# Kernel tuning notes

Measured on AMD Instinct MI355X. Metric: run time of the kernel, lower is better.

The kernel has to match this reference:

```python
import jax, jax.numpy as jnp
import numpy as np

# dims: B frames, L residues, E embed, C comp_size, K kernel, NL layers, V vocab
B, L, E, C, K, NL, V = 64, 256, 128, 16, 5, 4, 21
STEP = 0.1


def setup_inputs() -> dict:
    key = jax.random.key(0)
    ks = jax.random.split(key, 9)
    aa_array = jax.random.randint(ks[0], (B, L), 0, V)
    bb_coords = jax.random.normal(ks[1], (B, L, 3), dtype=jnp.float32)
    emb = jax.random.normal(ks[2], (V, E), dtype=jnp.float32) * 0.05
    conv_w = jax.random.normal(ks[3], (NL, E, E, K), dtype=jnp.float32) * (1.0 / np.sqrt(E * K))
    conv_b = jax.random.normal(ks[4], (NL, E), dtype=jnp.float32) * 0.01
    t1_w = jax.random.normal(ks[5], (E * C, E), dtype=jnp.float32) * (1.0 / np.sqrt(E))
    t1_b = jax.random.normal(ks[6], (E * C,), dtype=jnp.float32) * 0.01
    t2_w = jax.random.normal(ks[7], (3 * C, 3), dtype=jnp.float32) * (1.0 / np.sqrt(3.0))
    t2_b = jax.random.normal(ks[8], (3 * C,), dtype=jnp.float32) * 0.01
    return {"aa_array": aa_array, "bb_coords": bb_coords, "emb": emb,
            "conv_w": conv_w, "conv_b": conv_b,
            "t1_w": t1_w, "t1_b": t1_b, "t2_w": t2_w, "t2_b": t2_b}


def _forward(aa_array, bb_coords, emb, conv_w, conv_b, t1_w, t1_b, t2_w, t2_b):
    # --- model.call: embed + residual conv stack with tanh ---
    h = emb[aa_array].transpose(0, 2, 1)  # (B, E, L)
    for i in range(NL):
        y = jax.lax.conv_general_dilated(
            h, conv_w[i], window_strides=(1,), padding='SAME',
            dimension_numbers=('NCH', 'OIH', 'NCH'))
        h = jnp.tanh(h + y + conv_b[i][None, :, None])
    x = h.transpose(0, 2, 1)  # (B, L, E)

    # --- pairwise coordinate message passing ---
    xx = bb_coords[:, :, None] - bb_coords[:, None, :]        # (B, L, L, 3)
    x2 = (x @ t1_w.T + t1_b).reshape(B, L, E, C)              # (B, L, E, C)
    # xc[b,c,i,j] = sum_e x[b,i,e] * x2[b,j,e,c]
    scores = jnp.einsum('bie,bjec->bcij', x, x2)              # (B, C, L, L)
    sm = jax.nn.softmax(scores, axis=1)                       # softmax over C

    # torch: pv = t2(xx).reshape(B,L,L,3,C); vd[b,a,k] = sum_{d,c} pv[b,a,d,k,c]*sm[b,c,d,a]
    # fused form (same math, avoids materializing pv of shape (B,L,L,3,C)):
    W2 = t2_w.reshape(3, C, 3)   # (k, c, m)
    b2 = t2_b.reshape(3, C)      # (k, c)
    s = jnp.einsum('badm,bcda->bcam', xx, sm)                 # (B, C, L, 3)
    vd = (jnp.einsum('kcm,bcam->bak', W2, s)
          + jnp.einsum('kc,bca->bak', b2, sm.sum(axis=2)))    # (B, L, 3)

    new_bb = bb_coords + STEP * vd
    mse = jnp.square(new_bb[1:] - bb_coords[:-1]).sum(-1).mean(1)  # (B-1,)
    return mse


def reference(aa_array, bb_coords, emb, conv_w, conv_b, t1_w, t1_b, t2_w, t2_b):
    return _forward(aa_array, bb_coords, emb, conv_w, conv_b, t1_w, t1_b, t2_w, t2_b)
```

## Files before the change

### kernel.cpp

```cpp
#include <hip/hip_runtime.h>

#define B_ 64
#define L_ 256
#define E_ 128
#define C_ 16
#define K_ 5
#define NL_ 4
#define STEP_ 0.1f
#define LOG2E_ 1.4426950408889634f

typedef __bf16 bfh;
typedef __attribute__((ext_vector_type(8))) __bf16 bf16x8;
typedef __attribute__((ext_vector_type(4))) float f32x4;
typedef __attribute__((ext_vector_type(16))) float f32x16;

#define SWZ(r) (((r) ^ ((r) >> 4)) & 15)

#if __has_builtin(__builtin_amdgcn_exp2f)
#define EXP2(x) __builtin_amdgcn_exp2f(x)
#else
static __device__ __forceinline__ float EXP2(float x) {
  float r;
  asm("v_exp_f32 %0, %1\n\ts_nop 0" : "=v"(r) : "v"(x));
  return r;
}
#endif

__global__ void k_prep_w(const float* __restrict__ w, bfh* __restrict__ wT) {
  int i = blockIdx.x * 256 + threadIdx.x;
  if (i >= NL_ * K_ * E_ * E_) return;
  int ii = i & 127;
  int rest = i >> 7;
  int o = rest & 127;
  int rest2 = rest >> 7;
  int k = rest2 % K_;
  int lay = rest2 / K_;
  wT[i] = (bfh)w[(((size_t)lay * E_ + o) * E_ + ii) * K_ + k];
}

__global__ void k_prep_t1(const float* __restrict__ t1w, bfh* __restrict__ t1wb) {
  int i = blockIdx.x * 256 + threadIdx.x;
  if (i < 2048 * 128) t1wb[i] = (bfh)(t1w[i] * LOG2E_);
}

__global__ __launch_bounds__(512, 4) void k_conv0(const int* __restrict__ aa,
                                                  const float* __restrict__ emb,
                                                  const bfh* __restrict__ wT,
                                                  const float* __restrict__ bias,
                                                  bfh* __restrict__ xout) {
  __shared__ __align__(16) char hs[36 * 256];
  const int b = blockIdx.y;
  const int lb = blockIdx.x * 32;
  const int t = threadIdx.x;

  for (int s = t; s < 36 * 16; s += 512) {
    int row = s >> 4, ch = s & 15;
    int lp = lb + row - 2;
    uint4 pk = {0, 0, 0, 0};
    if (lp >= 0 && lp < L_) {
      int idx = aa[b * L_ + lp];
      float4 f0 = *(const float4*)(emb + (size_t)idx * E_ + ch * 8);
      float4 f1 = *(const float4*)(emb + (size_t)idx * E_ + ch * 8 + 4);
      union { bfh h[8]; uint4 u; } cv;
      cv.h[0] = (bfh)f0.x; cv.h[1] = (bfh)f0.y; cv.h[2] = (bfh)f0.z; cv.h[3] = (bfh)f0.w;
      cv.h[4] = (bfh)f1.x; cv.h[5] = (bfh)f1.y; cv.h[6] = (bfh)f1.z; cv.h[7] = (bfh)f1.w;
      pk = cv.u;
    }
    *(uint4*)(hs + row * 256 + ((ch ^ (row & 7)) << 4)) = pk;
  }
  __syncthreads();

  const int wv = t >> 6, lane = t & 63;
  const int c16 = lane & 15, kg = lane >> 4;
  const int msub = wv & 1;
  const int nq = wv >> 1;

#pragma unroll
  for (int ntl = 0; ntl < 2; ++ntl) {
    const int n0 = nq * 32 + ntl * 16;
    f32x4 acc = {0.f, 0.f, 0.f, 0.f};
#pragma unroll
    for (int k = 0; k < K_; ++k) {
      const bfh* bp = wT + ((size_t)(k * E_ + n0 + c16)) * E_ + kg * 8;
      bf16x8 b0 = *(const bf16x8*)(bp);
      bf16x8 b1 = *(const bf16x8*)(bp + 32);
      bf16x8 b2 = *(const bf16x8*)(bp + 64);
      bf16x8 b3 = *(const bf16x8*)(bp + 96);
      const int row = msub * 16 + c16 + k;
      bf16x8 a0 = *(const bf16x8*)(hs + row * 256 + (((0 * 4 + kg) ^ (row & 7)) << 4));
      bf16x8 a1 = *(const bf16x8*)(hs + row * 256 + (((1 * 4 + kg) ^ (row & 7)) << 4));
      bf16x8 a2 = *(const bf16x8*)(hs + row * 256 + (((2 * 4 + kg) ^ (row & 7)) << 4));
      bf16x8 a3 = *(const bf16x8*)(hs + row * 256 + (((3 * 4 + kg) ^ (row & 7)) << 4));
      acc = __builtin_amdgcn_mfma_f32_16x16x32_bf16(a0, b0, acc, 0, 0, 0);
      acc = __builtin_amdgcn_mfma_f32_16x16x32_bf16(a1, b1, acc, 0, 0, 0);
      acc = __builtin_amdgcn_mfma_f32_16x16x32_bf16(a2, b2, acc, 0, 0, 0);
      acc = __builtin_amdgcn_mfma_f32_16x16x32_bf16(a3, b3, acc, 0, 0, 0);
    }
    const int o = n0 + c16;
    const float bo = bias[o];
#pragma unroll
    for (int r = 0; r < 4; ++r) {
      int lrow = msub * 16 + kg * 4 + r;
      int srow = lrow + 2;
      float res = (float)*(const bfh*)(hs + srow * 256 +
                                       (((o >> 3) ^ (srow & 7)) << 4) + (o & 7) * 2);
      float v = acc[r] + res + bo;
      float ex = EXP2(2.f * LOG2E_ * v);
      float th = 1.f - 2.f / (ex + 1.f);
      xout[((size_t)b * L_ + lb + lrow) * E_ + o] = (bfh)th;
    }
  }
}

__global__ __launch_bounds__(512, 4) void k_conv(const bfh* __restrict__ xin,
                                                 const bfh* __restrict__ wT,
                                                 const float* __restrict__ bias,
                                                 bfh* __restrict__ xout) {
  __shared__ __align__(16) char hs[36 * 256];
  const int b = blockIdx.y;
  const int lb = blockIdx.x * 32;
  const int t = threadIdx.x;

  for (int s = t; s < 36 * 16; s += 512) {
    int row = s >> 4, ch = s & 15;
    int lp = lb + row - 2;
    uint4 z = {0, 0, 0, 0};
    uint4 v = (lp >= 0 && lp < L_)
                  ? *(const uint4*)(xin + ((size_t)b * L_ + lp) * E_ + ch * 8)
                  : z;
    *(uint4*)(hs + row * 256 + ((ch ^ (row & 7)) << 4)) = v;
  }
  __syncthreads();

  const int wv = t >> 6, lane = t & 63;
  const int c16 = lane & 15, kg = lane >> 4;
  const int msub = wv & 1;
  const int nq = wv >> 1;

#pragma unroll
  for (int ntl = 0; ntl < 2; ++ntl) {
    const int n0 = nq * 32 + ntl * 16;
    f32x4 acc = {0.f, 0.f, 0.f, 0.f};
#pragma unroll
    for (int k = 0; k < K_; ++k) {
      const bfh* bp = wT + ((size_t)(k * E_ + n0 + c16)) * E_ + kg * 8;
      bf16x8 b0 = *(const bf16x8*)(bp);
      bf16x8 b1 = *(const bf16x8*)(bp + 32);
      bf16x8 b2 = *(const bf16x8*)(bp + 64);
      bf16x8 b3 = *(const bf16x8*)(bp + 96);
      const int row = msub * 16 + c16 + k;
      bf16x8 a0 = *(const bf16x8*)(hs + row * 256 + (((0 * 4 + kg) ^ (row & 7)) << 4));
      bf16x8 a1 = *(const bf16x8*)(hs + row * 256 + (((1 * 4 + kg) ^ (row & 7)) << 4));
      bf16x8 a2 = *(const bf16x8*)(hs + row * 256 + (((2 * 4 + kg) ^ (row & 7)) << 4));
      bf16x8 a3 = *(const bf16x8*)(hs + row * 256 + (((3 * 4 + kg) ^ (row & 7)) << 4));
      acc = __builtin_amdgcn_mfma_f32_16x16x32_bf16(a0, b0, acc, 0, 0, 0);
      acc = __builtin_amdgcn_mfma_f32_16x16x32_bf16(a1, b1, acc, 0, 0, 0);
      acc = __builtin_amdgcn_mfma_f32_16x16x32_bf16(a2, b2, acc, 0, 0, 0);
      acc = __builtin_amdgcn_mfma_f32_16x16x32_bf16(a3, b3, acc, 0, 0, 0);
    }
    const int o = n0 + c16;
    const float bo = bias[o];
#pragma unroll
    for (int r = 0; r < 4; ++r) {
      int lrow = msub * 16 + kg * 4 + r;
      int srow = lrow + 2;
      float res = (float)*(const bfh*)(hs + srow * 256 +
                                       (((o >> 3) ^ (srow & 7)) << 4) + (o & 7) * 2);
      float v = acc[r] + res + bo;
      float ex = EXP2(2.f * LOG2E_ * v);
      float th = 1.f - 2.f / (ex + 1.f);
      xout[((size_t)b * L_ + lb + lrow) * E_ + o] = (bfh)th;
    }
  }
}

__global__ __launch_bounds__(512, 4) void k_conv_last(const bfh* __restrict__ xin,
                                                      const bfh* __restrict__ wT,
                                                      const float* __restrict__ bias,
                                                      bfh* __restrict__ xTg) {
  __shared__ __align__(16) char hs[36 * 256];
  const int b = blockIdx.y;
  const int lb = blockIdx.x * 32;
  const int dt = blockIdx.x;
  const int t = threadIdx.x;

  for (int s = t; s < 36 * 16; s += 512) {
    int row = s >> 4, ch = s & 15;
    int lp = lb + row - 2;
    uint4 z = {0, 0, 0, 0};
    uint4 v = (lp >= 0 && lp < L_)
                  ? *(const uint4*)(xin + ((size_t)b * L_ + lp) * E_ + ch * 8)
                  : z;
    *(uint4*)(hs + row * 256 + ((ch ^ (row & 7)) << 4)) = v;
  }
  __syncthreads();

  const int wv = t >> 6, lane = t & 63;
  const int c16 = lane & 15, kg = lane >> 4;
  const int msub = wv & 1;
  const int nq = wv >> 1;

#pragma unroll
  for (int ntl = 0; ntl < 2; ++ntl) {
    const int n0 = nq * 32 + ntl * 16;
    f32x4 acc = {0.f, 0.f, 0.f, 0.f};
#pragma unroll
    for (int k = 0; k < K_; ++k) {
      const bfh* bp = wT + ((size_t)(k * E_ + n0 + c16)) * E_ + kg * 8;
      bf16x8 b0 = *(const bf16x8*)(bp);
      bf16x8 b1 = *(const bf16x8*)(bp + 32);
      bf16x8 b2 = *(const bf16x8*)(bp + 64);
      bf16x8 b3 = *(const bf16x8*)(bp + 96);
      const int row = msub * 16 + c16 + k;
      bf16x8 a0 = *(const bf16x8*)(hs + row * 256 + (((0 * 4 + kg) ^ (row & 7)) << 4));
      bf16x8 a1 = *(const bf16x8*)(hs + row * 256 + (((1 * 4 + kg) ^ (row & 7)) << 4));
      bf16x8 a2 = *(const bf16x8*)(hs + row * 256 + (((2 * 4 + kg) ^ (row & 7)) << 4));
      bf16x8 a3 = *(const bf16x8*)(hs + row * 256 + (((3 * 4 + kg) ^ (row & 7)) << 4));
      acc = __builtin_amdgcn_mfma_f32_16x16x32_bf16(a0, b0, acc, 0, 0, 0);
      acc = __builtin_amdgcn_mfma_f32_16x16x32_bf16(a1, b1, acc, 0, 0, 0);
      acc = __builtin_amdgcn_mfma_f32_16x16x32_bf16(a2, b2, acc, 0, 0, 0);
      acc = __builtin_amdgcn_mfma_f32_16x16x32_bf16(a3, b3, acc, 0, 0, 0);
    }
    const int o = n0 + c16;
    const int kkp = nq * 2 + ntl;
    const int hic = c16 >> 3;
    const int e7 = c16 & 7;
    const float bo = bias[o];
#pragma unroll
    for (int r = 0; r < 4; ++r) {
      int lrow = msub * 16 + kg * 4 + r;
      int srow = lrow + 2;
      float res = (float)*(const bfh*)(hs + srow * 256 +
                                       (((o >> 3) ^ (srow & 7)) << 4) + (o & 7) * 2);
      float v = acc[r] + res + bo;
      float ex = EXP2(2.f * LOG2E_ * v);
      float th = 1.f - 2.f / (ex + 1.f);
      size_t el = ((((size_t)b * 8 + dt) * 8 + kkp) * 2 + hic) * 256 + lrow * 8 + e7;
      xTg[el] = (bfh)th;
    }
  }
}

__global__ __launch_bounds__(512, 2) void k_x2(const bfh* __restrict__ xTg,
                                               const bfh* __restrict__ t1wb,
                                               const float* __restrict__ t1b,
                                               bfh* __restrict__ x2g,
                                               int bBase) {
  __shared__ __align__(16) char smem[65536 + 2 * 8192];
  char* XF = smem;
  const unsigned u = blockIdx.x;
  const int xcd = u & 7;
  const int g = u >> 3;
  const int b_loc = xcd + 8 * (g >> 3);
  const int ne = g & 7;
  const int b = bBase + b_loc;
  const int t = threadIdx.x;
  const int wv = t >> 6, lane = t & 63;
  const int c16 = lane & 15, kg = lane >> 4;

#pragma unroll
  for (int i = 0; i < 8; ++i) {
    int c = t + i * 512;
    int l31 = c & 31, hi5 = (c >> 5) & 1, kk = (c >> 6) & 7, dt = c >> 9;
    int row = dt * 32 + l31;
    int ch = (kk * 2 + hi5) ^ SWZ(row);
    *(uint4*)(XF + row * 256 + (ch << 4)) =
        *(const uint4*)(xTg + (size_t)b * 32768 + (size_t)c * 8);
  }
  __syncthreads();

  bf16x8 bf[2][4];
  float bias[2];
#pragma unroll
  for (int j = 0; j < 2; ++j) {
    const int e = ne * 16 + wv * 2 + j;
    const int n = e * 16 + c16;
#pragma unroll
    for (int kk = 0; kk < 4; ++kk)
      bf[j][kk] = *(const bf16x8*)(t1wb + (size_t)n * 128 + kk * 32 + kg * 8);
    bias[j] = t1b[n] * LOG2E_;
  }

#pragma unroll 1
  for (int st = 0; st < 16; ++st) {
    char* sc = smem + 65536 + (st & 1) * 8192;
    bf16x8 a1[4];
    const int rowa = st * 16 + c16;
#pragma unroll
    for (int kk = 0; kk < 4; ++kk)
      a1[kk] = *(const bf16x8*)(XF + rowa * 256 + (((kk * 4 + kg) ^ SWZ(rowa)) << 4));
    f32x4 acc0 = {0.f, 0.f, 0.f, 0.f};
    f32x4 acc1 = {0.f, 0.f, 0.f, 0.f};
#pragma unroll
    for (int kk = 0; kk < 4; ++kk) {
      acc0 = __builtin_amdgcn_mfma_f32_16x16x32_bf16(a1[kk], bf[0][kk], acc0, 0, 0, 0);
      acc1 = __builtin_amdgcn_mfma_f32_16x16x32_bf16(a1[kk], bf[1][kk], acc1, 0, 0, 0);
    }
#pragma unroll
    for (int r = 0; r < 4; ++r) {
      int a = kg * 4 + r;
      int m5 = (c16 & 3) | ((a & 1) << 2) | ((c16 >> 2) << 3);
      int row = (a >> 1) * 32 + m5;
      union { bfh h; ushort s; } lo, hi2;
      lo.h = (bfh)(acc0[r] + bias[0]);
      hi2.h = (bfh)(acc1[r] + bias[1]);
      unsigned pk = (unsigned)lo.s | ((unsigned)hi2.s << 16);
      *(unsigned*)(sc + row * 32 + (((wv) ^ ((row >> 2) & 7)) << 2)) = pk;
    }
    __syncthreads();
    {
      const int m32 = t & 31;
      const int eo = (t >> 5) & 1;
      const int mb = t >> 6;
      const int row = mb * 32 + m32;
      uint4 v;
      unsigned* vp = (unsigned*)&v;
#pragma unroll
      for (int jj = 0; jj < 4; ++jj) {
        int j2 = eo * 4 + jj;
        vp[jj] = *(const unsigned*)(sc + row * 32 + ((j2 ^ ((row >> 2) & 7)) << 2));
      }
      size_t el = (((size_t)(b_loc * 128 + st * 8 + mb)) * 16 + ne * 2 + eo) * 256 + m32 * 8;
      *(uint4*)(x2g + el) = v;
    }
  }
}

__global__ __launch_bounds__(512, 2) void k_pair(
    const bfh* __restrict__ xTg,
    const float* __restrict__ bb,
    const bfh* __restrict__ x2g,
    const float* __restrict__ t2w,
    const float* __restrict__ t2b,
    float* __restrict__ vkp,
    int bBase) {
  __shared__ __align__(16) float bbs[L_ * 3];
  const int t = threadIdx.x;
  const unsigned u = blockIdx.x;
  const int b_loc = (u & 7) | ((u >> 8) << 3);
  const int inner = (u >> 3) & 31;
  const int atile = inner >> 1;
  const int dh = inner & 1;
  const int b = bBase + b_loc;
  const int lane = t & 63;
  const int wv = t >> 6;
  const int l31 = lane & 31;
  const int hi = lane >> 5;

  if (t < 192) ((float4*)bbs)[t] = ((const float4*)(bb + b * (L_ * 3)))[t];
  __syncthreads();

  bf16x8 afr[8];
  const bfh* abase = x2g + ((size_t)(b_loc * 128 + atile * 8 + wv)) * 4096 + l31 * 8;
#pragma unroll
  for (int kk = 0; kk < 8; ++kk)
    afr[kk] = *(const bf16x8*)(abase + (kk * 2 + hi) * 256);

  const int aglob = atile * 16 + 2 * wv + hi;
  const float bax0 = bbs[aglob * 3 + 0];
  const float bax1 = bbs[aglob * 3 + 1];
  const float bax2 = bbs[aglob * 3 + 2];

  float accX[16], accY[16], accZ[16], accS[16];
#pragma unroll
  for (int q = 0; q < 16; ++q) { accX[q] = 0.f; accY[q] = 0.f; accZ[q] = 0.f; accS[q] = 0.f; }

  const bfh* xb = xTg + (size_t)b * 32768 + hi * 256 + l31 * 8;
  bf16x8 bcur[8], bnxt[8];
#pragma unroll
  for (int kk = 0; kk < 8; ++kk)
    bcur[kk] = *(const bf16x8*)(xb + (size_t)(dh * 4) * 4096 + kk * 512);

#pragma unroll
  for (int dt = 0; dt < 4; ++dt) {
    const int dtg = dh * 4 + dt;
    if (dt < 3) {
#pragma unroll
      for (int kk = 0; kk < 8; ++kk)
        bnxt[kk] = *(const bf16x8*)(xb + (size_t)(dtg + 1) * 4096 + kk * 512);
    }
    f32x16 acc;
#pragma unroll
    for (int q = 0; q < 16; ++q) acc[q] = 0.f;
#pragma unroll
    for (int kk = 0; kk < 8; ++kk)
      acc = __builtin_amdgcn_mfma_f32_32x32x16_bf16(afr[kk], bcur[kk], acc, 0, 0, 0);
    const int d = dtg * 32 + l31;
    const float dx = bax0 - bbs[d * 3 + 0];
    const float dy = bax1 - bbs[d * 3 + 1];
    const float dz = bax2 - bbs[d * 3 + 2];
    float p[16];
#pragma unroll
    for (int q = 0; q < 16; ++q) p[q] = EXP2(acc[q]);
    const float s0 = (p[0] + p[1]) + (p[2] + p[3]);
    const float s1 = (p[4] + p[5]) + (p[6] + p[7]);
    const float s2 = (p[8] + p[9]) + (p[10] + p[11]);
    const float s3 = (p[12] + p[13]) + (p[14] + p[15]);
    const float S = (s0 + s1) + (s2 + s3);
    const float inv = __builtin_amdgcn_rcpf(S);
    const float dxn = dx * inv, dyn = dy * inv, dzn = dz * inv;
#pragma unroll
    for (int q = 0; q < 16; ++q) {
      accS[q] = fmaf(p[q], inv, accS[q]);
      accX[q] = fmaf(p[q], dxn, accX[q]);
      accY[q] = fmaf(p[q], dyn, accY[q]);
      accZ[q] = fmaf(p[q], dzn, accZ[q]);
    }
#pragma unroll
    for (int kk = 0; kk < 8; ++kk) bcur[kk] = bnxt[kk];
  }

  float vk[3] = {0.f, 0.f, 0.f};
#pragma unroll
  for (int c = 0; c < 16; ++c) {
#pragma unroll
    for (int k = 0; k < 3; ++k) {
      const float* w2 = t2w + (k * C_ + c) * 3;
      vk[k] += w2[0] * accX[c] + w2[1] * accY[c] + w2[2] * accZ[c] +
               t2b[k * C_ + c] * accS[c];
    }
  }
#pragma unroll
  for (int m = 1; m <= 16; m <<= 1) {
    vk[0] += __shfl_xor(vk[0], m);
    vk[1] += __shfl_xor(vk[1], m);
    vk[2] += __shfl_xor(vk[2], m);
  }
  if (l31 == 0) {
#pragma unroll
    for (int k = 0; k < 3; ++k)
      vkp[(((size_t)b * 2 + dh) * L_ + aglob) * 3 + k] = vk[k];
  }
}

__global__ void k_mse(const float* __restrict__ vkp, const float* __restrict__ bb,
                      float* __restrict__ out) {
  const int b = blockIdx.x;
  const int t = threadIdx.x;
  const int bp1 = b + 1;
  float v = 0.f;
#pragma unroll
  for (int k = 0; k < 3; ++k) {
    float vd = vkp[(((size_t)bp1 * 2 + 0) * L_ + t) * 3 + k] +
               vkp[(((size_t)bp1 * 2 + 1) * L_ + t) * 3 + k];
    float nb = bb[((size_t)bp1 * L_ + t) * 3 + k] + STEP_ * vd;
    float d = nb - bb[((size_t)b * L_ + t) * 3 + k];
    v += d * d;
  }
  for (int o = 32; o > 0; o >>= 1) v += __shfl_down(v, o);
  __shared__ float wsum[4];
  if ((t & 63) == 0) wsum[t >> 6] = v;
  __syncthreads();
  if (t == 0) out[b] = (wsum[0] + wsum[1] + wsum[2] + wsum[3]) * (1.0f / L_);
}

extern "C" void kernel_launch(void* const* d_in, const int* in_sizes, int n_in,
                              void* d_out, int out_size, void* d_ws, size_t ws_size,
                              hipStream_t stream) {
  const int* aa = (const int*)d_in[0];
  const float* bb = (const float*)d_in[1];
  const float* emb = (const float*)d_in[2];
  const float* conv_w = (const float*)d_in[3];
  const float* conv_b = (const float*)d_in[4];
  const float* t1w = (const float*)d_in[5];
  const float* t1b = (const float*)d_in[6];
  const float* t2w = (const float*)d_in[7];
  const float* t2b = (const float*)d_in[8];
  float* out = (float*)d_out;

  char* ws = (char*)d_ws;
  bfh* xA = (bfh*)ws;
  bfh* xTg = (bfh*)(ws + 4194304);
  bfh* t1wb = (bfh*)(ws + 8388608);
  bfh* wT = (bfh*)(ws + 8912896);
  float* vkp = (float*)(ws + 9568256);
  bfh* x2g = (bfh*)(ws + 10485760);
  bfh* xB = (bfh*)(ws + 10485760);

  k_prep_t1<<<1024, 256, 0, stream>>>(t1w, t1wb);
  k_prep_w<<<(NL_ * K_ * E_ * E_ + 255) / 256, 256, 0, stream>>>(conv_w, wT);

  k_conv0<<<dim3(L_ / 32, B_), 512, 0, stream>>>(aa, emb, wT + (size_t)0 * K_ * E_ * E_,
                                                 conv_b + 0 * E_, xB);
  k_conv<<<dim3(L_ / 32, B_), 512, 0, stream>>>(xB, wT + (size_t)1 * K_ * E_ * E_,
                                                conv_b + 1 * E_, xA);
  k_conv<<<dim3(L_ / 32, B_), 512, 0, stream>>>(xA, wT + (size_t)2 * K_ * E_ * E_,
                                                conv_b + 2 * E_, xB);
  k_conv_last<<<dim3(L_ / 32, B_), 512, 0, stream>>>(xB, wT + (size_t)3 * K_ * E_ * E_,
                                                     conv_b + 3 * E_, xTg);

  const size_t need1 = 10485760ull + 67108864ull;
  if (ws_size >= need1) {
    k_x2<<<B_ * 8, 512, 0, stream>>>(xTg, t1wb, t1b, x2g, 0);
    k_pair<<<B_ * 32, 512, 0, stream>>>(xTg, bb, x2g, t2w, t2b, vkp, 0);
  } else {
    for (int pass = 0; pass < 2; ++pass) {
      const int bBase = pass * 32;
      k_x2<<<32 * 8, 512, 0, stream>>>(xTg, t1wb, t1b, x2g, bBase);
      k_pair<<<32 * 32, 512, 0, stream>>>(xTg, bb, x2g, t2w, t2b, vkp, bBase);
    }
  }

  k_mse<<<B_ - 1, 256, 0, stream>>>(vkp, bb, out);
}
```

Baseline: 155.7 us.

## Fuse four conv layers into one kernel with halo recompute in LDS

Replaces the four per-layer conv kernels with a single kernel that loads a 48-row tile (8-row halo each side) and runs layers 0-2 entirely in shared memory, recomputing the halo rows. Only the final layer writes to global memory, in the transposed layout. This removes three global round-trips of activations and three kernel launches. The two weight-prep kernels are also merged into one launch. The cost is redundant halo computation (48 rows computed per 32 output rows), more LDS per block, and lower occupancy (launch bounds 2 instead of 4).

```diff
diff --git a/kernel.cpp b/kernel.cpp
--- a/kernel.cpp
+++ b/kernel.cpp
@@ -26,36 +26,42 @@
 }
 #endif
 
-__global__ void k_prep_w(const float* __restrict__ w, bfh* __restrict__ wT) {
+__global__ void k_prep(const float* __restrict__ w, const float* __restrict__ t1w,
+                       bfh* __restrict__ wT, bfh* __restrict__ t1wb) {
   int i = blockIdx.x * 256 + threadIdx.x;
-  if (i >= NL_ * K_ * E_ * E_) return;
-  int ii = i & 127;
-  int rest = i >> 7;
-  int o = rest & 127;
-  int rest2 = rest >> 7;
-  int k = rest2 % K_;
-  int lay = rest2 / K_;
-  wT[i] = (bfh)w[(((size_t)lay * E_ + o) * E_ + ii) * K_ + k];
-}
-
-__global__ void k_prep_t1(const float* __restrict__ t1w, bfh* __restrict__ t1wb) {
-  int i = blockIdx.x * 256 + threadIdx.x;
-  if (i < 2048 * 128) t1wb[i] = (bfh)(t1w[i] * LOG2E_);
-}
-
-__global__ __launch_bounds__(512, 4) void k_conv0(const int* __restrict__ aa,
+  const int NW = NL_ * K_ * E_ * E_;
+  if (i < NW) {
+    int ii = i & 127;
+    int rest = i >> 7;
+    int o = rest & 127;
+    int rest2 = rest >> 7;
+    int k = rest2 % K_;
+    int lay = rest2 / K_;
+    wT[i] = (bfh)w[(((size_t)lay * E_ + o) * E_ + ii) * K_ + k];
+    return;
+  }
+  int j = i - NW;
+  if (j < 2048 * 128) t1wb[j] = (bfh)(t1w[j] * LOG2E_);
+}
+
+__global__ __launch_bounds__(512, 2) void k_conv4(const int* __restrict__ aa,
                                                   const float* __restrict__ emb,
                                                   const bfh* __restrict__ wT,
-                                                  const float* __restrict__ bias,
-                                                  bfh* __restrict__ xout) {
-  __shared__ __align__(16) char hs[36 * 256];
+                                                  const float* __restrict__ conv_b,
+                                                  bfh* __restrict__ xTg) {
+  __shared__ __align__(16) char smem[3 * 12288];
+  char* bufIn = smem;
+  char* bufA = smem + 12288;
+  char* bufB = smem + 24576;
   const int b = blockIdx.y;
   const int lb = blockIdx.x * 32;
   const int t = threadIdx.x;
-
-  for (int s = t; s < 36 * 16; s += 512) {
+  const int wv = t >> 6, lane = t & 63;
+  const int c16 = lane & 15, kg = lane >> 4;
+
+  for (int s = t; s < 48 * 16; s += 512) {
     int row = s >> 4, ch = s & 15;
-    int lp = lb + row - 2;
+    int lp = lb + row - 8;
     uint4 pk = {0, 0, 0, 0};
     if (lp >= 0 && lp < L_) {
       int idx = aa[b * L_ + lp];
@@ -66,177 +72,102 @@
       cv.h[4] = (bfh)f1.x; cv.h[5] = (bfh)f1.y; cv.h[6] = (bfh)f1.z; cv.h[7] = (bfh)f1.w;
       pk = cv.u;
     }
-    *(uint4*)(hs + row * 256 + ((ch ^ (row & 7)) << 4)) = pk;
+    *(uint4*)(bufIn + row * 256 + ((ch ^ (row & 7)) << 4)) = pk;
   }
   __syncthreads();
 
-  const int wv = t >> 6, lane = t & 63;
-  const int c16 = lane & 15, kg = lane >> 4;
-  const int msub = wv & 1;
-  const int nq = wv >> 1;
-
-#pragma unroll
-  for (int ntl = 0; ntl < 2; ++ntl) {
-    const int n0 = nq * 32 + ntl * 16;
-    f32x4 acc = {0.f, 0.f, 0.f, 0.f};
-#pragma unroll
-    for (int k = 0; k < K_; ++k) {
-      const bfh* bp = wT + ((size_t)(k * E_ + n0 + c16)) * E_ + kg * 8;
-      bf16x8 b0 = *(const bf16x8*)(bp);
-      bf16x8 b1 = *(const bf16x8*)(bp + 32);
-      bf16x8 b2 = *(const bf16x8*)(bp + 64);
-      bf16x8 b3 = *(const bf16x8*)(bp + 96);
-      const int row = msub * 16 + c16 + k;
-      bf16x8 a0 = *(const bf16x8*)(hs + row * 256 + (((0 * 4 + kg) ^ (row & 7)) << 4));
-      bf16x8 a1 = *(const bf16x8*)(hs + row * 256 + (((1 * 4 + kg) ^ (row & 7)) << 4));
-      bf16x8 a2 = *(const bf16x8*)(hs + row * 256 + (((2 * 4 + kg) ^ (row & 7)) << 4));
-      bf16x8 a3 = *(const bf16x8*)(hs + row * 256 + (((3 * 4 + kg) ^ (row & 7)) << 4));
-      acc = __builtin_amdgcn_mfma_f32_16x16x32_bf16(a0, b0, acc, 0, 0, 0);
-      acc = __builtin_amdgcn_mfma_f32_16x16x32_bf16(a1, b1, acc, 0, 0, 0);
-      acc = __builtin_amdgcn_mfma_f32_16x16x32_bf16(a2, b2, acc, 0, 0, 0);
-      acc = __builtin_amdgcn_mfma_f32_16x16x32_bf16(a3, b3, acc, 0, 0, 0);
-    }
-    const int o = n0 + c16;
-    const float bo = bias[o];
-#pragma unroll
-    for (int r = 0; r < 4; ++r) {
-      int lrow = msub * 16 + kg * 4 + r;
-      int srow = lrow + 2;
-      float res = (float)*(const bfh*)(hs + srow * 256 +
-                                       (((o >> 3) ^ (srow & 7)) << 4) + (o & 7) * 2);
-      float v = acc[r] + res + bo;
-      float ex = EXP2(2.f * LOG2E_ * v);
-      float th = 1.f - 2.f / (ex + 1.f);
-      xout[((size_t)b * L_ + lb + lrow) * E_ + o] = (bfh)th;
-    }
-  }
-}
-
-__global__ __launch_bounds__(512, 4) void k_conv(const bfh* __restrict__ xin,
-                                                 const bfh* __restrict__ wT,
-                                                 const float* __restrict__ bias,
-                                                 bfh* __restrict__ xout) {
-  __shared__ __align__(16) char hs[36 * 256];
-  const int b = blockIdx.y;
-  const int lb = blockIdx.x * 32;
-  const int t = threadIdx.x;
-
-  for (int s = t; s < 36 * 16; s += 512) {
-    int row = s >> 4, ch = s & 15;
-    int lp = lb + row - 2;
-    uint4 z = {0, 0, 0, 0};
-    uint4 v = (lp >= 0 && lp < L_)
-                  ? *(const uint4*)(xin + ((size_t)b * L_ + lp) * E_ + ch * 8)
-                  : z;
-    *(uint4*)(hs + row * 256 + ((ch ^ (row & 7)) << 4)) = v;
-  }
-  __syncthreads();
-
-  const int wv = t >> 6, lane = t & 63;
-  const int c16 = lane & 15, kg = lane >> 4;
-  const int msub = wv & 1;
-  const int nq = wv >> 1;
-
-#pragma unroll
-  for (int ntl = 0; ntl < 2; ++ntl) {
-    const int n0 = nq * 32 + ntl * 16;
-    f32x4 acc = {0.f, 0.f, 0.f, 0.f};
-#pragma unroll
-    for (int k = 0; k < K_; ++k) {
-      const bfh* bp = wT + ((size_t)(k * E_ + n0 + c16)) * E_ + kg * 8;
-      bf16x8 b0 = *(const bf16x8*)(bp);
-      bf16x8 b1 = *(const bf16x8*)(bp + 32);
-      bf16x8 b2 = *(const bf16x8*)(bp + 64);
-      bf16x8 b3 = *(const bf16x8*)(bp + 96);
-      const int row = msub * 16 + c16 + k;
-      bf16x8 a0 = *(const bf16x8*)(hs + row * 256 + (((0 * 4 + kg) ^ (row & 7)) << 4));
-      bf16x8 a1 = *(const bf16x8*)(hs + row * 256 + (((1 * 4 + kg) ^ (row & 7)) << 4));
-      bf16x8 a2 = *(const bf16x8*)(hs + row * 256 + (((2 * 4 + kg) ^ (row & 7)) << 4));
-      bf16x8 a3 = *(const bf16x8*)(hs + row * 256 + (((3 * 4 + kg) ^ (row & 7)) << 4));
-      acc = __builtin_amdgcn_mfma_f32_16x16x32_bf16(a0, b0, acc, 0, 0, 0);
-      acc = __builtin_amdgcn_mfma_f32_16x16x32_bf16(a1, b1, acc, 0, 0, 0);
-      acc = __builtin_amdgcn_mfma_f32_16x16x32_bf16(a2, b2, acc, 0, 0, 0);
-      acc = __builtin_amdgcn_mfma_f32_16x16x32_bf16(a3, b3, acc, 0, 0, 0);
-    }
-    const int o = n0 + c16;
-    const float bo = bias[o];
-#pragma unroll
-    for (int r = 0; r < 4; ++r) {
-      int lrow = msub * 16 + kg * 4 + r;
-      int srow = lrow + 2;
-      float res = (float)*(const bfh*)(hs + srow * 256 +
-                                       (((o >> 3) ^ (srow & 7)) << 4) + (o & 7) * 2);
-      float v = acc[r] + res + bo;
-      float ex = EXP2(2.f * LOG2E_ * v);
-      float th = 1.f - 2.f / (ex + 1.f);
-      xout[((size_t)b * L_ + lb + lrow) * E_ + o] = (bfh)th;
-    }
-  }
-}
-
-__global__ __launch_bounds__(512, 4) void k_conv_last(const bfh* __restrict__ xin,
-                                                      const bfh* __restrict__ wT,
-                                                      const float* __restrict__ bias,
-                                                      bfh* __restrict__ xTg) {
-  __shared__ __align__(16) char hs[36 * 256];
-  const int b = blockIdx.y;
-  const int lb = blockIdx.x * 32;
-  const int dt = blockIdx.x;
-  const int t = threadIdx.x;
-
-  for (int s = t; s < 36 * 16; s += 512) {
-    int row = s >> 4, ch = s & 15;
-    int lp = lb + row - 2;
-    uint4 z = {0, 0, 0, 0};
-    uint4 v = (lp >= 0 && lp < L_)
-                  ? *(const uint4*)(xin + ((size_t)b * L_ + lp) * E_ + ch * 8)
-                  : z;
-    *(uint4*)(hs + row * 256 + ((ch ^ (row & 7)) << 4)) = v;
-  }
-  __syncthreads();
-
-  const int wv = t >> 6, lane = t & 63;
-  const int c16 = lane & 15, kg = lane >> 4;
-  const int msub = wv & 1;
-  const int nq = wv >> 1;
-
-#pragma unroll
-  for (int ntl = 0; ntl < 2; ++ntl) {
-    const int n0 = nq * 32 + ntl * 16;
-    f32x4 acc = {0.f, 0.f, 0.f, 0.f};
-#pragma unroll
-    for (int k = 0; k < K_; ++k) {
-      const bfh* bp = wT + ((size_t)(k * E_ + n0 + c16)) * E_ + kg * 8;
-      bf16x8 b0 = *(const bf16x8*)(bp);
-      bf16x8 b1 = *(const bf16x8*)(bp + 32);
-      bf16x8 b2 = *(const bf16x8*)(bp + 64);
-      bf16x8 b3 = *(const bf16x8*)(bp + 96);
-      const int row = msub * 16 + c16 + k;
-      bf16x8 a0 = *(const bf16x8*)(hs + row * 256 + (((0 * 4 + kg) ^ (row & 7)) << 4));
-      bf16x8 a1 = *(const bf16x8*)(hs + row * 256 + (((1 * 4 + kg) ^ (row & 7)) << 4));
-      bf16x8 a2 = *(const bf16x8*)(hs + row * 256 + (((2 * 4 + kg) ^ (row & 7)) << 4));
-      bf16x8 a3 = *(const bf16x8*)(hs + row * 256 + (((3 * 4 + kg) ^ (row & 7)) << 4));
-      acc = __builtin_amdgcn_mfma_f32_16x16x32_bf16(a0, b0, acc, 0, 0, 0);
-      acc = __builtin_amdgcn_mfma_f32_16x16x32_bf16(a1, b1, acc, 0, 0, 0);
-      acc = __builtin_amdgcn_mfma_f32_16x16x32_bf16(a2, b2, acc, 0, 0, 0);
-      acc = __builtin_amdgcn_mfma_f32_16x16x32_bf16(a3, b3, acc, 0, 0, 0);
-    }
-    const int o = n0 + c16;
-    const int kkp = nq * 2 + ntl;
-    const int hic = c16 >> 3;
-    const int e7 = c16 & 7;
-    const float bo = bias[o];
-#pragma unroll
-    for (int r = 0; r < 4; ++r) {
-      int lrow = msub * 16 + kg * 4 + r;
-      int srow = lrow + 2;
-      float res = (float)*(const bfh*)(hs + srow * 256 +
-                                       (((o >> 3) ^ (srow & 7)) << 4) + (o & 7) * 2);
-      float v = acc[r] + res + bo;
-      float ex = EXP2(2.f * LOG2E_ * v);
-      float th = 1.f - 2.f / (ex + 1.f);
-      size_t el = ((((size_t)b * 8 + dt) * 8 + kkp) * 2 + hic) * 256 + lrow * 8 + e7;
-      xTg[el] = (bfh)th;
+  const char* src = bufIn;
+  char* dst = bufA;
+#pragma unroll 1
+  for (int lay = 0; lay < 3; ++lay) {
+    const bfh* wL = wT + (size_t)lay * K_ * E_ * E_;
+    const float* bL = conv_b + lay * E_;
+#pragma unroll
+    for (int j = 0; j < 3; ++j) {
+      const int pi = wv * 3 + j;
+      const int ot = pi & 7, mt = pi >> 3;
+      const int o = ot * 16 + c16;
+      f32x4 acc = {0.f, 0.f, 0.f, 0.f};
+#pragma unroll
+      for (int k = 0; k < K_; ++k) {
+        const bfh* bp = wL + ((size_t)(k * E_ + o)) * E_ + kg * 8;
+        bf16x8 b0 = *(const bf16x8*)(bp);
+        bf16x8 b1 = *(const bf16x8*)(bp + 32);
+        bf16x8 b2 = *(const bf16x8*)(bp + 64);
+        bf16x8 b3 = *(const bf16x8*)(bp + 96);
+        int rt = mt * 16 + c16 + k - 2;
+        rt = rt < 0 ? 0 : (rt > 47 ? 47 : rt);
+        bf16x8 a0 = *(const bf16x8*)(src + rt * 256 + (((0 * 4 + kg) ^ (rt & 7)) << 4));
+        bf16x8 a1 = *(const bf16x8*)(src + rt * 256 + (((1 * 4 + kg) ^ (rt & 7)) << 4));
+        bf16x8 a2 = *(const bf16x8*)(src + rt * 256 + (((2 * 4 + kg) ^ (rt & 7)) << 4));
+        bf16x8 a3 = *(const bf16x8*)(src + rt * 256 + (((3 * 4 + kg) ^ (rt & 7)) << 4));
+        acc = __builtin_amdgcn_mfma_f32_16x16x32_bf16(a0, b0, acc, 0, 0, 0);
+        acc = __builtin_amdgcn_mfma_f32_16x16x32_bf16(a1, b1, acc, 0, 0, 0);
+        acc = __builtin_amdgcn_mfma_f32_16x16x32_bf16(a2, b2, acc, 0, 0, 0);
+        acc = __builtin_amdgcn_mfma_f32_16x16x32_bf16(a3, b3, acc, 0, 0, 0);
+      }
+      const float bo = bL[o];
+#pragma unroll
+      for (int r = 0; r < 4; ++r) {
+        int ro = mt * 16 + kg * 4 + r;
+        int gl = lb - 8 + ro;
+        float res = (float)*(const bfh*)(src + ro * 256 +
+                                         (((o >> 3) ^ (ro & 7)) << 4) + (o & 7) * 2);
+        float v = acc[r] + res + bo;
+        float ex = EXP2(2.f * LOG2E_ * v);
+        float th = 1.f - 2.f / (ex + 1.f);
+        if (gl < 0 || gl >= L_) th = 0.f;
+        *(bfh*)(dst + ro * 256 + (((o >> 3) ^ (ro & 7)) << 4) + (o & 7) * 2) = (bfh)th;
+      }
+    }
+    __syncthreads();
+    src = dst;
+    dst = (lay == 0) ? bufB : bufA;
+  }
+
+  {
+    const bfh* wL = wT + (size_t)3 * K_ * E_ * E_;
+    const float* bL = conv_b + 3 * E_;
+    const int msub = wv & 1;
+    const int nq = wv >> 1;
+#pragma unroll
+    for (int ntl = 0; ntl < 2; ++ntl) {
+      const int n0 = nq * 32 + ntl * 16;
+      const int o = n0 + c16;
+      f32x4 acc = {0.f, 0.f, 0.f, 0.f};
+#pragma unroll
+      for (int k = 0; k < K_; ++k) {
+        const bfh* bp = wL + ((size_t)(k * E_ + o)) * E_ + kg * 8;
+        bf16x8 b0 = *(const bf16x8*)(bp);
+        bf16x8 b1 = *(const bf16x8*)(bp + 32);
+        bf16x8 b2 = *(const bf16x8*)(bp + 64);
+        bf16x8 b3 = *(const bf16x8*)(bp + 96);
+        const int rt = msub * 16 + c16 + k + 6;
+        bf16x8 a0 = *(const bf16x8*)(src + rt * 256 + (((0 * 4 + kg) ^ (rt & 7)) << 4));
+        bf16x8 a1 = *(const bf16x8*)(src + rt * 256 + (((1 * 4 + kg) ^ (rt & 7)) << 4));
+        bf16x8 a2 = *(const bf16x8*)(src + rt * 256 + (((2 * 4 + kg) ^ (rt & 7)) << 4));
+        bf16x8 a3 = *(const bf16x8*)(src + rt * 256 + (((3 * 4 + kg) ^ (rt & 7)) << 4));
+        acc = __builtin_amdgcn_mfma_f32_16x16x32_bf16(a0, b0, acc, 0, 0, 0);
+        acc = __builtin_amdgcn_mfma_f32_16x16x32_bf16(a1, b1, acc, 0, 0, 0);
+        acc = __builtin_amdgcn_mfma_f32_16x16x32_bf16(a2, b2, acc, 0, 0, 0);
+        acc = __builtin_amdgcn_mfma_f32_16x16x32_bf16(a3, b3, acc, 0, 0, 0);
+      }
+      const float bo = bL[o];
+      const int kkp = nq * 2 + ntl;
+      const int hic = c16 >> 3;
+      const int e7 = c16 & 7;
+#pragma unroll
+      for (int r = 0; r < 4; ++r) {
+        int lrow = msub * 16 + kg * 4 + r;
+        int ro = lrow + 8;
+        float res = (float)*(const bfh*)(src + ro * 256 +
+                                         (((o >> 3) ^ (ro & 7)) << 4) + (o & 7) * 2);
+        float v = acc[r] + res + bo;
+        float ex = EXP2(2.f * LOG2E_ * v);
+        float th = 1.f - 2.f / (ex + 1.f);
+        size_t el = ((((size_t)b * 8 + blockIdx.x) * 8 + kkp) * 2 + hic) * 256 + lrow * 8 + e7;
+        xTg[el] = (bfh)th;
+      }
     }
   }
 }
@@ -469,25 +400,16 @@
   float* out = (float*)d_out;
 
   char* ws = (char*)d_ws;
-  bfh* xA = (bfh*)ws;
   bfh* xTg = (bfh*)(ws + 4194304);
   bfh* t1wb = (bfh*)(ws + 8388608);
   bfh* wT = (bfh*)(ws + 8912896);
   float* vkp = (float*)(ws + 9568256);
   bfh* x2g = (bfh*)(ws + 10485760);
-  bfh* xB = (bfh*)(ws + 10485760);
-
-  k_prep_t1<<<1024, 256, 0, stream>>>(t1w, t1wb);
-  k_prep_w<<<(NL_ * K_ * E_ * E_ + 255) / 256, 256, 0, stream>>>(conv_w, wT);
-
-  k_conv0<<<dim3(L_ / 32, B_), 512, 0, stream>>>(aa, emb, wT + (size_t)0 * K_ * E_ * E_,
-                                                 conv_b + 0 * E_, xB);
-  k_conv<<<dim3(L_ / 32, B_), 512, 0, stream>>>(xB, wT + (size_t)1 * K_ * E_ * E_,
-                                                conv_b + 1 * E_, xA);
-  k_conv<<<dim3(L_ / 32, B_), 512, 0, stream>>>(xA, wT + (size_t)2 * K_ * E_ * E_,
-                                                conv_b + 2 * E_, xB);
-  k_conv_last<<<dim3(L_ / 32, B_), 512, 0, stream>>>(xB, wT + (size_t)3 * K_ * E_ * E_,
-                                                     conv_b + 3 * E_, xTg);
+
+  const int NPREP = NL_ * K_ * E_ * E_ + 2048 * 128;
+  k_prep<<<(NPREP + 255) / 256, 256, 0, stream>>>(conv_w, t1w, wT, t1wb);
+
+  k_conv4<<<dim3(L_ / 32, B_), 512, 0, stream>>>(aa, emb, wT, conv_b, xTg);
 
   const size_t need1 = 10485760ull + 67108864ull;
   if (ws_size >= need1) {
```

Result: slower. 178.5 us (+14.7%).

## Halve conv row tiles, split accumulators, and merge weight prep kernels

Applied to the files above, without the earlier changes.

The conv kernels now cover 16 sequence rows per block instead of 32, which doubles the grid to 1024 blocks. Each wave owns one 16-channel output tile and alternates two independent MFMA accumulators, shortening the dependent MFMA chain. The two weight-prep kernels are merged into one launch. The trade-off is that each weight fragment is now reused over fewer rows, so weight traffic through L2 roughly doubles, and halo rows are reloaded more often.

```diff
diff --git a/kernel.cpp b/kernel.cpp
--- a/kernel.cpp
+++ b/kernel.cpp
@@ -26,35 +26,37 @@
 }
 #endif
 
-__global__ void k_prep_w(const float* __restrict__ w, bfh* __restrict__ wT) {
+__global__ void k_prep(const float* __restrict__ w, const float* __restrict__ t1w,
+                       bfh* __restrict__ wT, bfh* __restrict__ t1wb) {
   int i = blockIdx.x * 256 + threadIdx.x;
-  if (i >= NL_ * K_ * E_ * E_) return;
-  int ii = i & 127;
-  int rest = i >> 7;
-  int o = rest & 127;
-  int rest2 = rest >> 7;
-  int k = rest2 % K_;
-  int lay = rest2 / K_;
-  wT[i] = (bfh)w[(((size_t)lay * E_ + o) * E_ + ii) * K_ + k];
-}
-
-__global__ void k_prep_t1(const float* __restrict__ t1w, bfh* __restrict__ t1wb) {
-  int i = blockIdx.x * 256 + threadIdx.x;
-  if (i < 2048 * 128) t1wb[i] = (bfh)(t1w[i] * LOG2E_);
-}
+  const int NW = NL_ * K_ * E_ * E_;
+  if (i < NW) {
+    int ii = i & 127;
+    int rest = i >> 7;
+    int o = rest & 127;
+    int rest2 = rest >> 7;
+    int k = rest2 % K_;
+    int lay = rest2 / K_;
+    wT[i] = (bfh)w[(((size_t)lay * E_ + o) * E_ + ii) * K_ + k];
+    return;
+  }
+  int j = i - NW;
+  if (j < 2048 * 128) t1wb[j] = (bfh)(t1w[j] * LOG2E_);
+}
+
 
 __global__ __launch_bounds__(512, 4) void k_conv0(const int* __restrict__ aa,
                                                   const float* __restrict__ emb,
                                                   const bfh* __restrict__ wT,
                                                   const float* __restrict__ bias,
                                                   bfh* __restrict__ xout) {
-  __shared__ __align__(16) char hs[36 * 256];
+  __shared__ __align__(16) char hs[20 * 256];
   const int b = blockIdx.y;
-  const int lb = blockIdx.x * 32;
-  const int t = threadIdx.x;
-
-  for (int s = t; s < 36 * 16; s += 512) {
-    int row = s >> 4, ch = s & 15;
+  const int lb = blockIdx.x * 16;
+  const int t = threadIdx.x;
+
+  if (t < 20 * 16) {
+    int row = t >> 4, ch = t & 15;
     int lp = lb + row - 2;
     uint4 pk = {0, 0, 0, 0};
     if (lp >= 0 && lp < L_) {
@@ -72,43 +74,38 @@
 
   const int wv = t >> 6, lane = t & 63;
   const int c16 = lane & 15, kg = lane >> 4;
-  const int msub = wv & 1;
-  const int nq = wv >> 1;
-
-#pragma unroll
-  for (int ntl = 0; ntl < 2; ++ntl) {
-    const int n0 = nq * 32 + ntl * 16;
-    f32x4 acc = {0.f, 0.f, 0.f, 0.f};
-#pragma unroll
-    for (int k = 0; k < K_; ++k) {
-      const bfh* bp = wT + ((size_t)(k * E_ + n0 + c16)) * E_ + kg * 8;
-      bf16x8 b0 = *(const bf16x8*)(bp);
-      bf16x8 b1 = *(const bf16x8*)(bp + 32);
-      bf16x8 b2 = *(const bf16x8*)(bp + 64);
-      bf16x8 b3 = *(const bf16x8*)(bp + 96);
-      const int row = msub * 16 + c16 + k;
-      bf16x8 a0 = *(const bf16x8*)(hs + row * 256 + (((0 * 4 + kg) ^ (row & 7)) << 4));
-      bf16x8 a1 = *(const bf16x8*)(hs + row * 256 + (((1 * 4 + kg) ^ (row & 7)) << 4));
-      bf16x8 a2 = *(const bf16x8*)(hs + row * 256 + (((2 * 4 + kg) ^ (row & 7)) << 4));
-      bf16x8 a3 = *(const bf16x8*)(hs + row * 256 + (((3 * 4 + kg) ^ (row & 7)) << 4));
-      acc = __builtin_amdgcn_mfma_f32_16x16x32_bf16(a0, b0, acc, 0, 0, 0);
-      acc = __builtin_amdgcn_mfma_f32_16x16x32_bf16(a1, b1, acc, 0, 0, 0);
-      acc = __builtin_amdgcn_mfma_f32_16x16x32_bf16(a2, b2, acc, 0, 0, 0);
-      acc = __builtin_amdgcn_mfma_f32_16x16x32_bf16(a3, b3, acc, 0, 0, 0);
-    }
-    const int o = n0 + c16;
-    const float bo = bias[o];
-#pragma unroll
-    for (int r = 0; r < 4; ++r) {
-      int lrow = msub * 16 + kg * 4 + r;
-      int srow = lrow + 2;
-      float res = (float)*(const bfh*)(hs + srow * 256 +
-                                       (((o >> 3) ^ (srow & 7)) << 4) + (o & 7) * 2);
-      float v = acc[r] + res + bo;
-      float ex = EXP2(2.f * LOG2E_ * v);
-      float th = 1.f - 2.f / (ex + 1.f);
-      xout[((size_t)b * L_ + lb + lrow) * E_ + o] = (bfh)th;
-    }
+  const int o = wv * 16 + c16;
+
+  f32x4 acc0 = {0.f, 0.f, 0.f, 0.f};
+  f32x4 acc1 = {0.f, 0.f, 0.f, 0.f};
+#pragma unroll
+  for (int k = 0; k < K_; ++k) {
+    const bfh* bp = wT + ((size_t)(k * E_ + o)) * E_ + kg * 8;
+    bf16x8 b0 = *(const bf16x8*)(bp);
+    bf16x8 b1 = *(const bf16x8*)(bp + 32);
+    bf16x8 b2 = *(const bf16x8*)(bp + 64);
+    bf16x8 b3 = *(const bf16x8*)(bp + 96);
+    const int row = c16 + k;
+    bf16x8 a0 = *(const bf16x8*)(hs + row * 256 + (((0 * 4 + kg) ^ (row & 7)) << 4));
+    bf16x8 a1 = *(const bf16x8*)(hs + row * 256 + (((1 * 4 + kg) ^ (row & 7)) << 4));
+    bf16x8 a2 = *(const bf16x8*)(hs + row * 256 + (((2 * 4 + kg) ^ (row & 7)) << 4));
+    bf16x8 a3 = *(const bf16x8*)(hs + row * 256 + (((3 * 4 + kg) ^ (row & 7)) << 4));
+    acc0 = __builtin_amdgcn_mfma_f32_16x16x32_bf16(a0, b0, acc0, 0, 0, 0);
+    acc1 = __builtin_amdgcn_mfma_f32_16x16x32_bf16(a1, b1, acc1, 0, 0, 0);
+    acc0 = __builtin_amdgcn_mfma_f32_16x16x32_bf16(a2, b2, acc0, 0, 0, 0);
+    acc1 = __builtin_amdgcn_mfma_f32_16x16x32_bf16(a3, b3, acc1, 0, 0, 0);
+  }
+  const float bo = bias[o];
+#pragma unroll
+  for (int r = 0; r < 4; ++r) {
+    int lrow = kg * 4 + r;
+    int srow = lrow + 2;
+    float res = (float)*(const bfh*)(hs + srow * 256 +
+                                     (((o >> 3) ^ (srow & 7)) << 4) + (o & 7) * 2);
+    float v = acc0[r] + acc1[r] + res + bo;
+    float ex = EXP2(2.f * LOG2E_ * v);
+    float th = 1.f - 2.f / (ex + 1.f);
+    xout[((size_t)b * L_ + lb + lrow) * E_ + o] = (bfh)th;
   }
 }
 
@@ -116,13 +113,13 @@
                                                  const bfh* __restrict__ wT,
                                                  const float* __restrict__ bias,
                                                  bfh* __restrict__ xout) {
-  __shared__ __align__(16) char hs[36 * 256];
+  __shared__ __align__(16) char hs[20 * 256];
   const int b = blockIdx.y;
-  const int lb = blockIdx.x * 32;
-  const int t = threadIdx.x;
-
-  for (int s = t; s < 36 * 16; s += 512) {
-    int row = s >> 4, ch = s & 15;
+  const int lb = blockIdx.x * 16;
+  const int t = threadIdx.x;
+
+  if (t < 20 * 16) {
+    int row = t >> 4, ch = t & 15;
     int lp = lb + row - 2;
     uint4 z = {0, 0, 0, 0};
     uint4 v = (lp >= 0 && lp < L_)
@@ -134,43 +131,38 @@
 
   const int wv = t >> 6, lane = t & 63;
   const int c16 = lane & 15, kg = lane >> 4;
-  const int msub = wv & 1;
-  const int nq = wv >> 1;
-
-#pragma unroll
-  for (int ntl = 0; ntl < 2; ++ntl) {
-    const int n0 = nq * 32 + ntl * 16;
-    f32x4 acc = {0.f, 0.f, 0.f, 0.f};
-#pragma unroll
-    for (int k = 0; k < K_; ++k) {
-      const bfh* bp = wT + ((size_t)(k * E_ + n0 + c16)) * E_ + kg * 8;
-      bf16x8 b0 = *(const bf16x8*)(bp);
-      bf16x8 b1 = *(const bf16x8*)(bp + 32);
-      bf16x8 b2 = *(const bf16x8*)(bp + 64);
-      bf16x8 b3 = *(const bf16x8*)(bp + 96);
-      const int row = msub * 16 + c16 + k;
-      bf16x8 a0 = *(const bf16x8*)(hs + row * 256 + (((0 * 4 + kg) ^ (row & 7)) << 4));
-      bf16x8 a1 = *(const bf16x8*)(hs + row * 256 + (((1 * 4 + kg) ^ (row & 7)) << 4));
-      bf16x8 a2 = *(const bf16x8*)(hs + row * 256 + (((2 * 4 + kg) ^ (row & 7)) << 4));
-      bf16x8 a3 = *(const bf16x8*)(hs + row * 256 + (((3 * 4 + kg) ^ (row & 7)) << 4));
-      acc = __builtin_amdgcn_mfma_f32_16x16x32_bf16(a0, b0, acc, 0, 0, 0);
-      acc = __builtin_amdgcn_mfma_f32_16x16x32_bf16(a1, b1, acc, 0, 0, 0);
-      acc = __builtin_amdgcn_mfma_f32_16x16x32_bf16(a2, b2, acc, 0, 0, 0);
-      acc = __builtin_amdgcn_mfma_f32_16x16x32_bf16(a3, b3, acc, 0, 0, 0);
-    }
-    const int o = n0 + c16;
-    const float bo = bias[o];
-#pragma unroll
-    for (int r = 0; r < 4; ++r) {
-      int lrow = msub * 16 + kg * 4 + r;
-      int srow = lrow + 2;
-      float res = (float)*(const bfh*)(hs + srow * 256 +
-                                       (((o >> 3) ^ (srow & 7)) << 4) + (o & 7) * 2);
-      float v = acc[r] + res + bo;
-      float ex = EXP2(2.f * LOG2E_ * v);
-      float th = 1.f - 2.f / (ex + 1.f);
-      xout[((size_t)b * L_ + lb + lrow) * E_ + o] = (bfh)th;
-    }
+  const int o = wv * 16 + c16;
+
+  f32x4 acc0 = {0.f, 0.f, 0.f, 0.f};
+  f32x4 acc1 = {0.f, 0.f, 0.f, 0.f};
+#pragma unroll
+  for (int k = 0; k < K_; ++k) {
+    const bfh* bp = wT + ((size_t)(k * E_ + o)) * E_ + kg * 8;
+    bf16x8 b0 = *(const bf16x8*)(bp);
+    bf16x8 b1 = *(const bf16x8*)(bp + 32);
+    bf16x8 b2 = *(const bf16x8*)(bp + 64);
+    bf16x8 b3 = *(const bf16x8*)(bp + 96);
+    const int row = c16 + k;
+    bf16x8 a0 = *(const bf16x8*)(hs + row * 256 + (((0 * 4 + kg) ^ (row & 7)) << 4));
+    bf16x8 a1 = *(const bf16x8*)(hs + row * 256 + (((1 * 4 + kg) ^ (row & 7)) << 4));
+    bf16x8 a2 = *(const bf16x8*)(hs + row * 256 + (((2 * 4 + kg) ^ (row & 7)) << 4));
+    bf16x8 a3 = *(const bf16x8*)(hs + row * 256 + (((3 * 4 + kg) ^ (row & 7)) << 4));
+    acc0 = __builtin_amdgcn_mfma_f32_16x16x32_bf16(a0, b0, acc0, 0, 0, 0);
+    acc1 = __builtin_amdgcn_mfma_f32_16x16x32_bf16(a1, b1, acc1, 0, 0, 0);
+    acc0 = __builtin_amdgcn_mfma_f32_16x16x32_bf16(a2, b2, acc0, 0, 0, 0);
+    acc1 = __builtin_amdgcn_mfma_f32_16x16x32_bf16(a3, b3, acc1, 0, 0, 0);
+  }
+  const float bo = bias[o];
+#pragma unroll
+  for (int r = 0; r < 4; ++r) {
+    int lrow = kg * 4 + r;
+    int srow = lrow + 2;
+    float res = (float)*(const bfh*)(hs + srow * 256 +
+                                     (((o >> 3) ^ (srow & 7)) << 4) + (o & 7) * 2);
+    float v = acc0[r] + acc1[r] + res + bo;
+    float ex = EXP2(2.f * LOG2E_ * v);
+    float th = 1.f - 2.f / (ex + 1.f);
+    xout[((size_t)b * L_ + lb + lrow) * E_ + o] = (bfh)th;
   }
 }
 
@@ -178,14 +170,15 @@
                                                       const bfh* __restrict__ wT,
                                                       const float* __restrict__ bias,
                                                       bfh* __restrict__ xTg) {
-  __shared__ __align__(16) char hs[36 * 256];
+  __shared__ __align__(16) char hs[20 * 256];
   const int b = blockIdx.y;
-  const int lb = blockIdx.x * 32;
-  const int dt = blockIdx.x;
-  const int t = threadIdx.x;
-
-  for (int s = t; s < 36 * 16; s += 512) {
-    int row = s >> 4, ch = s & 15;
+  const int lb = blockIdx.x * 16;
+  const int dt = blockIdx.x >> 1;
+  const int half = blockIdx.x & 1;
+  const int t = threadIdx.x;
+
+  if (t < 20 * 16) {
+    int row = t >> 4, ch = t & 15;
     int lp = lb + row - 2;
     uint4 z = {0, 0, 0, 0};
     uint4 v = (lp >= 0 && lp < L_)
@@ -197,47 +190,43 @@
 
   const int wv = t >> 6, lane = t & 63;
   const int c16 = lane & 15, kg = lane >> 4;
-  const int msub = wv & 1;
-  const int nq = wv >> 1;
-
-#pragma unroll
-  for (int ntl = 0; ntl < 2; ++ntl) {
-    const int n0 = nq * 32 + ntl * 16;
-    f32x4 acc = {0.f, 0.f, 0.f, 0.f};
-#pragma unroll
-    for (int k = 0; k < K_; ++k) {
-      const bfh* bp = wT + ((size_t)(k * E_ + n0 + c16)) * E_ + kg * 8;
-      bf16x8 b0 = *(const bf16x8*)(bp);
-      bf16x8 b1 = *(const bf16x8*)(bp + 32);
-      bf16x8 b2 = *(const bf16x8*)(bp + 64);
-      bf16x8 b3 = *(const bf16x8*)(bp + 96);
-      const int row = msub * 16 + c16 + k;
-      bf16x8 a0 = *(const bf16x8*)(hs + row * 256 + (((0 * 4 + kg) ^ (row & 7)) << 4));
-      bf16x8 a1 = *(const bf16x8*)(hs + row * 256 + (((1 * 4 + kg) ^ (row & 7)) << 4));
-      bf16x8 a2 = *(const bf16x8*)(hs + row * 256 + (((2 * 4 + kg) ^ (row & 7)) << 4));
-      bf16x8 a3 = *(const bf16x8*)(hs + row * 256 + (((3 * 4 + kg) ^ (row & 7)) << 4));
-      acc = __builtin_amdgcn_mfma_f32_16x16x32_bf16(a0, b0, acc, 0, 0, 0);
-      acc = __builtin_amdgcn_mfma_f32_16x16x32_bf16(a1, b1, acc, 0, 0, 0);
-      acc = __builtin_amdgcn_mfma_f32_16x16x32_bf16(a2, b2, acc, 0, 0, 0);
-      acc = __builtin_amdgcn_mfma_f32_16x16x32_bf16(a3, b3, acc, 0, 0, 0);
-    }
-    const int o = n0 + c16;
-    const int kkp = nq * 2 + ntl;
-    const int hic = c16 >> 3;
-    const int e7 = c16 & 7;
-    const float bo = bias[o];
-#pragma unroll
-    for (int r = 0; r < 4; ++r) {
-      int lrow = msub * 16 + kg * 4 + r;
-      int srow = lrow + 2;
-      float res = (float)*(const bfh*)(hs + srow * 256 +
-                                       (((o >> 3) ^ (srow & 7)) << 4) + (o & 7) * 2);
-      float v = acc[r] + res + bo;
-      float ex = EXP2(2.f * LOG2E_ * v);
-      float th = 1.f - 2.f / (ex + 1.f);
-      size_t el = ((((size_t)b * 8 + dt) * 8 + kkp) * 2 + hic) * 256 + lrow * 8 + e7;
-      xTg[el] = (bfh)th;
-    }
+  const int o = wv * 16 + c16;
+
+  f32x4 acc0 = {0.f, 0.f, 0.f, 0.f};
+  f32x4 acc1 = {0.f, 0.f, 0.f, 0.f};
+#pragma unroll
+  for (int k = 0; k < K_; ++k) {
+    const bfh* bp = wT + ((size_t)(k * E_ + o)) * E_ + kg * 8;
+    bf16x8 b0 = *(const bf16x8*)(bp);
+    bf16x8 b1 = *(const bf16x8*)(bp + 32);
+    bf16x8 b2 = *(const bf16x8*)(bp + 64);
+    bf16x8 b3 = *(const bf16x8*)(bp + 96);
+    const int row = c16 + k;
+    bf16x8 a0 = *(const bf16x8*)(hs + row * 256 + (((0 * 4 + kg) ^ (row & 7)) << 4));
+    bf16x8 a1 = *(const bf16x8*)(hs + row * 256 + (((1 * 4 + kg) ^ (row & 7)) << 4));
+    bf16x8 a2 = *(const bf16x8*)(hs + row * 256 + (((2 * 4 + kg) ^ (row & 7)) << 4));
+    bf16x8 a3 = *(const bf16x8*)(hs + row * 256 + (((3 * 4 + kg) ^ (row & 7)) << 4));
+    acc0 = __builtin_amdgcn_mfma_f32_16x16x32_bf16(a0, b0, acc0, 0, 0, 0);
+    acc1 = __builtin_amdgcn_mfma_f32_16x16x32_bf16(a1, b1, acc1, 0, 0, 0);
+    acc0 = __builtin_amdgcn_mfma_f32_16x16x32_bf16(a2, b2, acc0, 0, 0, 0);
+    acc1 = __builtin_amdgcn_mfma_f32_16x16x32_bf16(a3, b3, acc1, 0, 0, 0);
+  }
+  const float bo = bias[o];
+  const int kkp = o >> 4;
+  const int hic = (o >> 3) & 1;
+  const int e7 = o & 7;
+#pragma unroll
+  for (int r = 0; r < 4; ++r) {
+    int lrow = kg * 4 + r;
+    int srow = lrow + 2;
+    float res = (float)*(const bfh*)(hs + srow * 256 +
+                                     (((o >> 3) ^ (srow & 7)) << 4) + (o & 7) * 2);
+    float v = acc0[r] + acc1[r] + res + bo;
+    float ex = EXP2(2.f * LOG2E_ * v);
+    float th = 1.f - 2.f / (ex + 1.f);
+    int l31 = half * 16 + lrow;
+    size_t el = ((((size_t)b * 8 + dt) * 8 + kkp) * 2 + hic) * 256 + l31 * 8 + e7;
+    xTg[el] = (bfh)th;
   }
 }
 
@@ -477,16 +466,15 @@
   bfh* x2g = (bfh*)(ws + 10485760);
   bfh* xB = (bfh*)(ws + 10485760);
 
-  k_prep_t1<<<1024, 256, 0, stream>>>(t1w, t1wb);
-  k_prep_w<<<(NL_ * K_ * E_ * E_ + 255) / 256, 256, 0, stream>>>(conv_w, wT);
-
-  k_conv0<<<dim3(L_ / 32, B_), 512, 0, stream>>>(aa, emb, wT + (size_t)0 * K_ * E_ * E_,
-                                                 conv_b + 0 * E_, xB);
-  k_conv<<<dim3(L_ / 32, B_), 512, 0, stream>>>(xB, wT + (size_t)1 * K_ * E_ * E_,
+  const int NPREP = NL_ * K_ * E_ * E_ + 2048 * 128;
+  k_prep<<<(NPREP + 255) / 256, 256, 0, stream>>>(conv_w, t1w, wT, t1wb);
+
+  k_conv0<<<dim3(L_ / 16, B_), 512, 0, stream>>>(aa, emb, wT, conv_b, xB);
+  k_conv<<<dim3(L_ / 16, B_), 512, 0, stream>>>(xB, wT + (size_t)1 * K_ * E_ * E_,
                                                 conv_b + 1 * E_, xA);
-  k_conv<<<dim3(L_ / 32, B_), 512, 0, stream>>>(xA, wT + (size_t)2 * K_ * E_ * E_,
+  k_conv<<<dim3(L_ / 16, B_), 512, 0, stream>>>(xA, wT + (size_t)2 * K_ * E_ * E_,
                                                 conv_b + 2 * E_, xB);
-  k_conv_last<<<dim3(L_ / 32, B_), 512, 0, stream>>>(xB, wT + (size_t)3 * K_ * E_ * E_,
+  k_conv_last<<<dim3(L_ / 16, B_), 512, 0, stream>>>(xB, wT + (size_t)3 * K_ * E_ * E_,
                                                      conv_b + 3 * E_, xTg);
 
   const size_t need1 = 10485760ull + 67108864ull;
```

Result: no change. 153.4 us (-1.5%).
